# Performance work log

Measured on AMD Instinct MI355X. Metric: run time of the kernel, lower is better.

The kernel has to match this reference:

```python
import jax, jax.numpy as jnp
import numpy as np

N_USERS = 70000
N_ITEMS = 30000
N_NODES = N_USERS + N_ITEMS
R = 3          # n_relations (hard-coded to 3 in original forward)
D = 64         # emb_dim
L = 2          # n_layers
E = 1_600_000  # nnz per relation adjacency


def setup_inputs() -> dict:
    key = jax.random.key(0)
    ks = jax.random.split(key, 11)
    s = 0.05  # xavier-ish scale
    return {
        'user_emb': jax.random.normal(ks[0], (N_USERS, D), jnp.float32) * s,
        'item_emb': jax.random.normal(ks[1], (N_ITEMS, D), jnp.float32) * s,
        'rel_emb':  jax.random.normal(ks[2], (R, D), jnp.float32) * s,
        'W_gc':     jax.random.normal(ks[3], (L, D, D), jnp.float32) * s,
        'W_rel':    jax.random.normal(ks[4], (L, D, D), jnp.float32) * s,
        'gru_w':    jax.random.normal(ks[5], (R, D, D), jnp.float32) * s,
        'gru_b':    jax.random.normal(ks[6], (R, D), jnp.float32) * s,
        'tra':      jax.random.normal(ks[7], (2, 2 * D), jnp.float32) * s,
        # normalized sparse adjacency values (~1/degree)
        'adj_vals': jax.random.uniform(ks[8], (R, E), jnp.float32) / 16.0,
        'adj_rows': jax.random.randint(ks[9], (R, E), 0, N_NODES, dtype=jnp.int32),
        'adj_cols': jax.random.randint(ks[10], (R, E), 0, N_NODES, dtype=jnp.int32),
    }


def reference(user_emb, item_emb, rel_emb, W_gc, W_rel, gru_w, gru_b, tra,
              adj_vals, adj_rows, adj_cols):
    # ego: [N, R, D] (same embedding replicated per relation channel)
    ego = jnp.broadcast_to(
        jnp.concatenate([user_emb, item_emb], axis=0)[:, None, :],
        (N_NODES, R, D))
    all_emb = ego
    rela = [rel_emb]  # per-layer relation embeddings [R, D]
    inv_sqrt = 1.0 / jnp.sqrt(jnp.float32(128.0))  # hard-coded in source

    for k in range(L):
        embs = []
        for i in range(R):  # small fixed relation loop
            # sparse adj @ ego[:, i, :] via gather + segment_sum
            msgs = ego[adj_cols[i], i, :] * adj_vals[i][:, None]        # [E, D]
            prop = jax.ops.segment_sum(msgs, adj_rows[i],
                                       num_segments=N_NODES)           # [N, D]
            embs.append(jax.nn.leaky_relu((prop * rela[k][i]) @ W_gc[k]))
        est = jnp.stack(embs, axis=1)                                   # [N, R, D]
        att = jax.nn.softmax(
            jnp.einsum('nrd,nsd->nrs', est, est) * inv_sqrt, axis=2)
        ego = jnp.einsum('nrs,nsd->nrd', att, est)
        # dropout rate 0.0 (eval) -> identity
        all_emb = all_emb + ego
        rela.append(rela[k] @ W_rel[k])

    att = jax.nn.softmax(jnp.einsum('nrd,nsd->nrs', all_emb, all_emb), axis=2)
    mid = jnp.einsum('nrs,nsd->nrd', att, all_emb)
    final = jnp.stack([all_emb[:, 0, :], all_emb[:, 1, :], mid[:, -1, :]],
                      axis=1) / (L + 1)                                  # [N, 3, D]
    u = final[:N_USERS]
    i_emb = jnp.concatenate(
        [final[N_USERS:], jnp.zeros((1, R, D), final.dtype)], axis=0)

    aux1 = u[:, 0, :] * (u[:, 0, :] @ gru_w[0] + gru_b[0])
    aux2 = u[:, 1, :] * (u[:, 1, :] @ gru_w[1] + gru_b[1])
    tgt = u[:, 2, :] * (u[:, 2, :] @ gru_w[2] + gru_b[2])
    score1 = jnp.concatenate([tgt, aux1], axis=1) @ tra[0]               # [N_u]
    score2 = jnp.concatenate([tgt, aux2], axis=1) @ tra[1]               # [N_u]

    rela_out = jnp.mean(jnp.stack(rela, axis=0), axis=0)                 # [R, D]
    return (u, i_emb, rela_out, score1, score2)
```

## Files before the change

### kernel.cpp

```cpp
#include <hip/hip_runtime.h>
#include <hip/hip_bf16.h>

#define N_USERS 70000
#define N_ITEMS 30000
#define N_NODES 100000
#define RD 192
#define EE 1600000
#define NE3 4800000
#define M3 300000
#define NSUB 98
#define NBUCK 294

#define OFF_U    0
#define OFF_I    13440000
#define OFF_IZ   19200000
#define OFF_RELA 19200192
#define OFF_S1   19200384
#define OFF_S2   19270384

typedef __hip_bfloat16 bf16;
typedef unsigned long long u64;
typedef __attribute__((ext_vector_type(8))) short short8;
typedef __attribute__((ext_vector_type(8))) unsigned short ushort8;
typedef __attribute__((ext_vector_type(4))) float f32x4;

__device__ __forceinline__ float b2f(bf16 v) { return __bfloat162float(v); }

union bfbits { bf16 b; unsigned short u; };

__device__ __forceinline__ float bits2f(unsigned short u) {
  bfbits x; x.u = u; return b2f(x.b);
}
__device__ __forceinline__ unsigned short f2bits(float f) {
  bfbits x; x.b = __float2bfloat16(f); return x.u;
}

__device__ __forceinline__ float loadf(const void* p, int i, bool f32) {
  return f32 ? ((const float*)p)[i] : b2f(((const bf16*)p)[i]);
}
__device__ __forceinline__ void storef(void* p, int i, float v, bool f32) {
  if (f32) ((float*)p)[i] = v;
  else ((bf16*)p)[i] = __float2bfloat16(v);
}

template <int NV>
__device__ __forceinline__ void wave_sum_n(float* v) {
#pragma unroll
  for (int off = 32; off >= 1; off >>= 1) {
    float t[NV];
#pragma unroll
    for (int k = 0; k < NV; ++k) t[k] = __shfl_xor(v[k], off, 64);
#pragma unroll
    for (int k = 0; k < NV; ++k) v[k] += t[k];
  }
}

__global__ void detect_kernel(const unsigned short* __restrict__ ue,
                              int* __restrict__ flag) {
  __shared__ int s;
  int t = threadIdx.x;
  if (t == 0) s = 0;
  __syncthreads();
  int big = 0;
  for (int j = t; j < 8192; j += 256) {
    int e = (ue[j] >> 7) & 0xFF;
    if (e >= 127) big = 1;
  }
  if (big) atomicOr(&s, 1);
  __syncthreads();
  if (t == 0) *flag = s;
}

__global__ void zero_row_kernel(void* out, const int* __restrict__ flag) {
  bool f32 = *flag != 0;
  storef(out, OFF_IZ + (int)threadIdx.x, 0.f, f32);
}

__global__ void rela_kernel(const void* __restrict__ rel_emb,
                            const void* __restrict__ W_rel,
                            const int* __restrict__ flag,
                            float* __restrict__ rela_f, void* out) {
  bool f32 = *flag != 0;
  __shared__ float r0s[192], r1s[192];
  int t = threadIdx.x;
  int i = t >> 6, d = t & 63;
  float r0 = loadf(rel_emb, t, f32);
  r0s[t] = r0;
  __syncthreads();
  float acc = 0.f;
  for (int k = 0; k < 64; ++k)
    acc += r0s[i * 64 + k] * loadf(W_rel, k * 64 + d, f32);
  r1s[t] = acc;
  __syncthreads();
  float acc2 = 0.f;
  for (int k = 0; k < 64; ++k)
    acc2 += r1s[i * 64 + k] * loadf(W_rel, 4096 + k * 64 + d, f32);
  rela_f[t] = r0;
  rela_f[192 + t] = acc;
  rela_f[384 + t] = acc2;
  storef(out, OFF_RELA + t, (r0 + acc + acc2) * (1.f / 3.f), f32);
}

__global__ __launch_bounds__(256) void init_kernel(
    const void* __restrict__ user_emb, const void* __restrict__ item_emb,
    const int* __restrict__ flag, bf16* __restrict__ ego0) {
  bool f32 = *flag != 0;
  int idx4 = blockIdx.x * 256 + threadIdx.x;
  if (idx4 >= N_NODES * RD / 4) return;
  int idx = idx4 << 2;
  int n = idx / RD;
  int rd = idx - n * RD;
  int d = rd & 63;
  const void* src;
  int off;
  if (n < N_USERS) { src = user_emb; off = n * 64 + d; }
  else             { src = item_emb; off = (n - N_USERS) * 64 + d; }
  ushort4 o;
  if (f32) {
    float4 fv = *(const float4*)((const float*)src + off);
    o.x = f2bits(fv.x); o.y = f2bits(fv.y); o.z = f2bits(fv.z); o.w = f2bits(fv.w);
  } else {
    o = *(const ushort4*)((const unsigned short*)src + off);
  }
  *(ushort4*)(ego0 + idx) = o;
}

__global__ __launch_bounds__(256) void bhist_kernel(
    const int* __restrict__ rows, int* __restrict__ bcnt) {
  __shared__ int h[NBUCK];
  int t = threadIdx.x;
  for (int j = t; j < NBUCK; j += 256) h[j] = 0;
  __syncthreads();
  int base = blockIdx.x * 4096;
  int m = min(4096, NE3 - base);
  for (int j = t; j < m; j += 256) {
    int idx = base + j;
    int i = idx / EE;
    int r = rows[idx];
    atomicAdd(&h[i * NSUB + (r >> 10)], 1);
  }
  __syncthreads();
  for (int j = t; j < NBUCK; j += 256)
    if (h[j]) atomicAdd(&bcnt[j], h[j]);
}

__global__ __launch_bounds__(512) void bscan_kernel(
    const int* __restrict__ bcnt, int* __restrict__ gcursor,
    int* __restrict__ bbase) {
  __shared__ int s[512];
  int t = threadIdx.x;
  int x = (t < NBUCK) ? bcnt[t] : 0;
  s[t] = x;
  __syncthreads();
  for (int off = 1; off < 512; off <<= 1) {
    int y = (t >= off) ? s[t - off] : 0;
    __syncthreads();
    s[t] += y;
    __syncthreads();
  }
  if (t < NBUCK) {
    int e = s[t] - x;
    gcursor[t] = e;
    bbase[t] = e;
  }
}

__global__ __launch_bounds__(256) void passA_kernel(
    const int* __restrict__ rows, const int* __restrict__ cols,
    const void* __restrict__ vals, const int* __restrict__ flag,
    int* __restrict__ gcursor, u64* __restrict__ abuf) {
  bool f32 = *flag != 0;
  __shared__ u64 pk[4096];
  __shared__ unsigned short bk[4096];
  __shared__ int cnt[NBUCK], pos[NBUCK], gbase[NBUCK];
  int t = threadIdx.x;
  for (int j = t; j < NBUCK; j += 256) { cnt[j] = 0; pos[j] = 0; }
  __syncthreads();
  int base = blockIdx.x * 4096;
  int m = min(4096, NE3 - base);
  for (int j = t; j < m; j += 256) {
    int idx = base + j;
    int i = idx / EE;
    int r = rows[idx];
    int c = cols[idx];
    unsigned short vb =
        f32 ? f2bits(((const float*)vals)[idx])
            : ((const unsigned short*)vals)[idx];
    int sub = r >> 10;
    int b = i * NSUB + sub;
    pk[j] = ((u64)(r & 1023) << 48) | ((u64)(unsigned)c << 16) | vb;
    bk[j] = (unsigned short)b;
    atomicAdd(&cnt[b], 1);
  }
  __syncthreads();
  for (int j = t; j < NBUCK; j += 256)
    if (cnt[j] > 0) gbase[j] = atomicAdd(&gcursor[j], cnt[j]);
  __syncthreads();
  for (int j = t; j < m; j += 256) {
    int b = bk[j];
    int p = atomicAdd(&pos[b], 1);
    abuf[gbase[b] + p] = pk[j];
  }
}

__global__ __launch_bounds__(256) void passB_kernel(
    const u64* __restrict__ abuf, const int* __restrict__ bbase,
    const int* __restrict__ bcnt, int* __restrict__ offs,
    int* __restrict__ counts, int2* __restrict__ sedge) {
  __shared__ int hist[1024];
  __shared__ int s[256];
  int b = blockIdx.x;
  int rel = b / NSUB, sub = b - rel * NSUB;
  int r0 = sub << 10;
  int nr = min(1024, N_NODES - r0);
  int gi = rel * N_NODES + r0;
  int t = threadIdx.x;
  for (int j = t; j < 1024; j += 256) hist[j] = 0;
  __syncthreads();
  int start = bbase[b];
  int cnt = bcnt[b];
  int end = start + cnt;
  for (int e = start + t; e < end; e += 256)
    atomicAdd(&hist[(int)(abuf[e] >> 48)], 1);
  __syncthreads();
  int j0 = t << 2;
  int a0 = hist[j0], a1 = hist[j0 + 1], a2 = hist[j0 + 2], a3 = hist[j0 + 3];
  int lsum = a0 + a1 + a2 + a3;
  s[t] = lsum;
  __syncthreads();
  for (int off = 1; off < 256; off <<= 1) {
    int y = (t >= off) ? s[t - off] : 0;
    __syncthreads();
    s[t] += y;
    __syncthreads();
  }
  int o0 = start + s[t] - lsum;
  int o1 = o0 + a0, o2 = o1 + a1, o3 = o2 + a2;
  hist[j0] = o0; hist[j0 + 1] = o1; hist[j0 + 2] = o2; hist[j0 + 3] = o3;
  if (j0 < nr) {
    *(int4*)(offs + gi + j0) = make_int4(o0, o1, o2, o3);
    *(int4*)(counts + gi + j0) = make_int4(a0, a1, a2, a3);
  }
  __syncthreads();
  int rbase = rel * 128;
  for (int e = start + t; e < end; e += 256) {
    u64 w = abuf[e];
    int rowlo = (int)(w >> 48);
    int c = (int)((w >> 16) & 0x3FFFF);
    float v = bits2f((unsigned short)(w & 0xFFFF));
    int p = atomicAdd(&hist[rowlo], 1);
    int2 eo; eo.x = c * 384 + rbase; eo.y = __float_as_int(v);
    sedge[p] = eo;
  }
}

__global__ __launch_bounds__(256, 8) void gather_kernel(
    const int2* __restrict__ sedge, const int* __restrict__ counts,
    const int* __restrict__ offs, const bf16* __restrict__ ego,
    bf16* __restrict__ prop) {
  int wave = threadIdx.x >> 6;
  int n = blockIdx.x * 4 + wave;
  int rel = blockIdx.y;
  int seg = rel * N_NODES + n;
  int lane = threadIdx.x & 63;
  int g = lane >> 3;
  int d8 = lane & 7;
  unsigned voff = (unsigned)(d8 << 4);
  int base = __builtin_amdgcn_readfirstlane(offs[seg]);
  int cnt = __builtin_amdgcn_readfirstlane(counts[seg]);
  const char* egob = (const char*)ego;
  float a0 = 0.f, a1 = 0.f, a2 = 0.f, a3 = 0.f;
  float a4 = 0.f, a5 = 0.f, a6 = 0.f, a7 = 0.f;
#define ACCUM(dv, vv)                                          \
  do {                                                         \
    a0 = fmaf(__int_as_float((dv).x << 16), (vv), a0);         \
    a1 = fmaf(__int_as_float((dv).x & 0xffff0000u), (vv), a1); \
    a2 = fmaf(__int_as_float((dv).y << 16), (vv), a2);         \
    a3 = fmaf(__int_as_float((dv).y & 0xffff0000u), (vv), a3); \
    a4 = fmaf(__int_as_float((dv).z << 16), (vv), a4);         \
    a5 = fmaf(__int_as_float((dv).z & 0xffff0000u), (vv), a5); \
    a6 = fmaf(__int_as_float((dv).w << 16), (vv), a6);         \
    a7 = fmaf(__int_as_float((dv).w & 0xffff0000u), (vv), a7); \
  } while (0)
  int cm = cnt - 1;
  int nb = (cnt + 15) >> 4;
  int j = 0;
  if (nb & 1) {
    int iA = min(g, cm), iB = min(8 + g, cm);
    int2 h0 = sedge[base + iA];
    int2 h1 = sedge[base + iB];
    uint4 dA = *(const uint4*)(egob + ((unsigned)h0.x + voff));
    uint4 dB = *(const uint4*)(egob + ((unsigned)h1.x + voff));
    float v0 = (g < cnt) ? __int_as_float(h0.y) : 0.f;
    float v1 = (8 + g < cnt) ? __int_as_float(h1.y) : 0.f;
    ACCUM(dA, v0);
    ACCUM(dB, v1);
    j = 16;
  }
  int e16 = nb << 4;
  for (; j < e16; j += 32) {
    int iA0 = min(j + g, cm),      iB0 = min(j + 8 + g, cm);
    int iA1 = min(j + 16 + g, cm), iB1 = min(j + 24 + g, cm);
    int2 h0a = sedge[base + iA0];
    int2 h1a = sedge[base + iB0];
    int2 h0b = sedge[base + iA1];
    int2 h1b = sedge[base + iB1];
    uint4 dA = *(const uint4*)(egob + ((unsigned)h0a.x + voff));
    uint4 dB = *(const uint4*)(egob + ((unsigned)h1a.x + voff));
    uint4 dC = *(const uint4*)(egob + ((unsigned)h0b.x + voff));
    uint4 dD = *(const uint4*)(egob + ((unsigned)h1b.x + voff));
    float v0 = (j + g < cnt) ? __int_as_float(h0a.y) : 0.f;
    float v1 = (j + 8 + g < cnt) ? __int_as_float(h1a.y) : 0.f;
    float v2 = (j + 16 + g < cnt) ? __int_as_float(h0b.y) : 0.f;
    float v3 = (j + 24 + g < cnt) ? __int_as_float(h1b.y) : 0.f;
    ACCUM(dA, v0);
    ACCUM(dB, v1);
    ACCUM(dC, v2);
    ACCUM(dD, v3);
  }
#undef ACCUM
#pragma unroll
  for (int off = 8; off <= 32; off <<= 1) {
    a0 += __shfl_xor(a0, off, 64);
    a1 += __shfl_xor(a1, off, 64);
    a2 += __shfl_xor(a2, off, 64);
    a3 += __shfl_xor(a3, off, 64);
    a4 += __shfl_xor(a4, off, 64);
    a5 += __shfl_xor(a5, off, 64);
    a6 += __shfl_xor(a6, off, 64);
    a7 += __shfl_xor(a7, off, 64);
  }
  if (g == 0) {
    uint4 o;
    o.x = (unsigned)f2bits(a0) | ((unsigned)f2bits(a1) << 16);
    o.y = (unsigned)f2bits(a2) | ((unsigned)f2bits(a3) << 16);
    o.z = (unsigned)f2bits(a4) | ((unsigned)f2bits(a5) << 16);
    o.w = (unsigned)f2bits(a6) | ((unsigned)f2bits(a7) << 16);
    *(uint4*)((char*)prop + (size_t)(n * RD + rel * 64) * 2 + voff) = o;
  }
}

__device__ __forceinline__ float attn_row(float a, float b, float c,
                                          float e0, float e1, float e2) {
  float m = fmaxf(a, fmaxf(b, c));
  float w0 = __expf(a - m), w1 = __expf(b - m), w2 = __expf(c - m);
  float inv = 1.f / (w0 + w1 + w2);
  return (w0 * e0 + w1 * e1 + w2 * e2) * inv;
}

__global__ __launch_bounds__(256, 4) void transform_attn_kernel(
    const bf16* __restrict__ prop, const float* __restrict__ rela_k,
    const void* __restrict__ Wgc, int wgc_off, const int* __restrict__ flag,
    bf16* __restrict__ ego_out) {
  bool f32 = *flag != 0;
  __shared__ __align__(16) unsigned short est_t[64 * 198];
  int t = threadIdx.x, lane = t & 63, wave = t >> 6;
  int quad = lane >> 4, m = lane & 15;
  int wcol = wave * 16 + m;
  short8 b0, b1;
#pragma unroll
  for (int j = 0; j < 8; ++j) {
    int k0 = quad * 8 + j;
    b0[j] = (short)f2bits(loadf(Wgc, wgc_off + k0 * 64 + wcol, f32));
    b1[j] = (short)f2bits(loadf(Wgc, wgc_off + (k0 + 32) * 64 + wcol, f32));
  }
  float relv0[16], relv1[16], relv2[16];
#pragma unroll
  for (int j = 0; j < 8; ++j) {
    int k0 = quad * 8 + j;
    relv0[j] = rela_k[k0];        relv0[8 + j] = rela_k[32 + k0];
    relv1[j] = rela_k[64 + k0];   relv1[8 + j] = rela_k[96 + k0];
    relv2[j] = rela_k[128 + k0];  relv2[8 + j] = rela_k[160 + k0];
  }
  int n0 = blockIdx.x * 64;
  int row0 = n0 * 3;
#pragma unroll
  for (int tr = 0; tr < 12; ++tr) {
    int rl = tr * 16 + m;
    int row = row0 + rl;
    int row_c = row < M3 ? row : 0;
    int i = rl % 3;
    const ushort8* pp = (const ushort8*)(prop + (size_t)row_c * 64 + quad * 8);
    ushort8 x0 = pp[0];
    ushort8 x1 = pp[4];
    short8 a0, a1;
#pragma unroll
    for (int j = 0; j < 8; ++j) {
      float r0 = (i == 0) ? relv0[j] : (i == 1 ? relv1[j] : relv2[j]);
      float r1 = (i == 0) ? relv0[8 + j] : (i == 1 ? relv1[8 + j] : relv2[8 + j]);
      a0[j] = (short)f2bits(bits2f(x0[j]) * r0);
      a1[j] = (short)f2bits(bits2f(x1[j]) * r1);
    }
    f32x4 acc = {0.f, 0.f, 0.f, 0.f};
    acc = __builtin_amdgcn_mfma_f32_16x16x32_bf16(a0, b0, acc, 0, 0, 0);
    acc = __builtin_amdgcn_mfma_f32_16x16x32_bf16(a1, b1, acc, 0, 0, 0);
    float v0 = acc[0]; v0 = v0 > 0.f ? v0 : 0.01f * v0;
    float v1 = acc[1]; v1 = v1 > 0.f ? v1 : 0.01f * v1;
    float v2 = acc[2]; v2 = v2 > 0.f ? v2 : 0.01f * v2;
    float v3 = acc[3]; v3 = v3 > 0.f ? v3 : 0.01f * v3;
    unsigned w0 = (unsigned)f2bits(v0) | ((unsigned)f2bits(v1) << 16);
    unsigned w1 = (unsigned)f2bits(v2) | ((unsigned)f2bits(v3) << 16);
    unsigned* p32 = (unsigned*)(est_t + wcol * 198 + tr * 16 + quad * 4);
    p32[0] = w0; p32[1] = w1;
  }
  __syncthreads();
  const float sc = 0.088388347648318447f;
  for (int jj = 0; jj < 16; ++jj) {
    int nl = wave * 16 + jj;
    int n = n0 + nl;
    if (n >= N_NODES) break;
    int rb = lane * 198 + 3 * nl;
    float e0 = bits2f(est_t[rb]);
    float e1 = bits2f(est_t[rb + 1]);
    float e2 = bits2f(est_t[rb + 2]);
    float s[6];
    s[0] = e0 * e0; s[1] = e0 * e1; s[2] = e0 * e2;
    s[3] = e1 * e1; s[4] = e1 * e2; s[5] = e2 * e2;
    wave_sum_n<6>(s);
    float o0 = attn_row(s[0] * sc, s[1] * sc, s[2] * sc, e0, e1, e2);
    float o1 = attn_row(s[1] * sc, s[3] * sc, s[4] * sc, e0, e1, e2);
    float o2 = attn_row(s[2] * sc, s[4] * sc, s[5] * sc, e0, e1, e2);
    int base = n * RD + lane;
    ego_out[base] = __float2bfloat16(o0);
    ego_out[base + 64] = __float2bfloat16(o1);
    ego_out[base + 128] = __float2bfloat16(o2);
  }
}

__global__ __launch_bounds__(256, 5) void final_kernel(
    const bf16* __restrict__ ego0, const bf16* __restrict__ ego1,
    const bf16* __restrict__ ego2, const void* __restrict__ gru_w,
    const void* __restrict__ gru_b, const void* __restrict__ tra,
    const int* __restrict__ flag, void* out) {
  bool f32 = *flag != 0;
  __shared__ __align__(16) unsigned short fmatu[192 * 72];
  __shared__ float sc_lds[128];
  int t = threadIdx.x, lane = t & 63, wave = t >> 6;
  int quad = lane >> 4, m = lane & 15;
  int wcol = wave * 16 + m;
  if (t < 128) sc_lds[t] = 0.f;
  short8 bw[3][2];
#pragma unroll
  for (int i = 0; i < 3; ++i)
#pragma unroll
    for (int j = 0; j < 8; ++j) {
      int k0 = quad * 8 + j;
      bw[i][0][j] = (short)f2bits(loadf(gru_w, i * 4096 + k0 * 64 + wcol, f32));
      bw[i][1][j] =
          (short)f2bits(loadf(gru_w, i * 4096 + (k0 + 32) * 64 + wcol, f32));
    }
  float bias0 = loadf(gru_b, wcol, f32);
  float bias1 = loadf(gru_b, 64 + wcol, f32);
  float bias2 = loadf(gru_b, 128 + wcol, f32);
  float ts0 = loadf(tra, wcol, f32);
  float ts1 = loadf(tra, 64 + wcol, f32);
  float ts2 = loadf(tra, 128 + wcol, f32);
  float ts3 = loadf(tra, 192 + wcol, f32);

  int n0 = blockIdx.x * 64;
  for (int jj = 0; jj < 16; jj += 2) {
    int nlA = wave * 16 + jj;
    int nlB = nlA + 1;
    int nA = n0 + nlA, nB = n0 + nlB;
    float a0A = 0.f, a1A = 0.f, a2A = 0.f;
    float a0B = 0.f, a1B = 0.f, a2B = 0.f;
    if (nA < N_NODES) {
      int bi = nA * RD + lane;
      a0A = b2f(ego0[bi]) + b2f(ego1[bi]) + b2f(ego2[bi]);
      a1A = b2f(ego0[bi + 64]) + b2f(ego1[bi + 64]) + b2f(ego2[bi + 64]);
      a2A = b2f(ego0[bi + 128]) + b2f(ego1[bi + 128]) + b2f(ego2[bi + 128]);
    }
    if (nB < N_NODES) {
      int bi = nB * RD + lane;
      a0B = b2f(ego0[bi]) + b2f(ego1[bi]) + b2f(ego2[bi]);
      a1B = b2f(ego0[bi + 64]) + b2f(ego1[bi + 64]) + b2f(ego2[bi + 64]);
      a2B = b2f(ego0[bi + 128]) + b2f(ego1[bi + 128]) + b2f(ego2[bi + 128]);
    }
    float s[6];
    s[0] = a2A * a0A; s[1] = a2A * a1A; s[2] = a2A * a2A;
    s[3] = a2B * a0B; s[4] = a2B * a1B; s[5] = a2B * a2B;
    wave_sum_n<6>(s);
    float mid2A = attn_row(s[0], s[1], s[2], a0A, a1A, a2A);
    float mid2B = attn_row(s[3], s[4], s[5], a0B, a1B, a2B);
    float f0A = a0A * (1.f / 3.f), f1A = a1A * (1.f / 3.f),
          f2A = mid2A * (1.f / 3.f);
    float f0B = a0B * (1.f / 3.f), f1B = a1B * (1.f / 3.f),
          f2B = mid2B * (1.f / 3.f);
    if (nA < N_NODES) {
      int ob = (nA < N_USERS) ? (OFF_U + nA * RD + lane)
                              : (OFF_I + (nA - N_USERS) * RD + lane);
      storef(out, ob, f0A, f32);
      storef(out, ob + 64, f1A, f32);
      storef(out, ob + 128, f2A, f32);
    }
    if (nB < N_NODES) {
      int ob = (nB < N_USERS) ? (OFF_U + nB * RD + lane)
                              : (OFF_I + (nB - N_USERS) * RD + lane);
      storef(out, ob, f0B, f32);
      storef(out, ob + 64, f1B, f32);
      storef(out, ob + 128, f2B, f32);
    }
    fmatu[(0 * 64 + nlA) * 72 + lane] = f2bits(f0A);
    fmatu[(1 * 64 + nlA) * 72 + lane] = f2bits(f1A);
    fmatu[(2 * 64 + nlA) * 72 + lane] = f2bits(f2A);
    fmatu[(0 * 64 + nlB) * 72 + lane] = f2bits(f0B);
    fmatu[(1 * 64 + nlB) * 72 + lane] = f2bits(f1B);
    fmatu[(2 * 64 + nlB) * 72 + lane] = f2bits(f2B);
  }
  __syncthreads();
  float p1a[4][4], p2a[4][4];
#pragma unroll
  for (int tr = 0; tr < 4; ++tr)
#pragma unroll
    for (int r = 0; r < 4; ++r) { p1a[tr][r] = 0.f; p2a[tr][r] = 0.f; }
#pragma unroll
  for (int i = 0; i < 3; ++i) {
    float bias = (i == 0) ? bias0 : (i == 1 ? bias1 : bias2);
#pragma unroll
    for (int tr = 0; tr < 4; ++tr) {
      int arow = (i * 64 + tr * 16 + m) * 72;
      short8 a0 = *(const short8*)(fmatu + arow + quad * 8);
      short8 a1 = *(const short8*)(fmatu + arow + 32 + quad * 8);
      f32x4 acc = {0.f, 0.f, 0.f, 0.f};
      acc = __builtin_amdgcn_mfma_f32_16x16x32_bf16(a0, bw[i][0], acc, 0, 0, 0);
      acc = __builtin_amdgcn_mfma_f32_16x16x32_bf16(a1, bw[i][1], acc, 0, 0, 0);
#pragma unroll
      for (int r = 0; r < 4; ++r) {
        int nl = tr * 16 + quad * 4 + r;
        float y = acc[r] + bias;
        float f = bits2f(fmatu[(i * 64 + nl) * 72 + wcol]);
        float prod = f * y;
        if (i == 0) p1a[tr][r] += prod * ts1;
        else if (i == 1) p2a[tr][r] += prod * ts3;
        else { p1a[tr][r] += prod * ts0; p2a[tr][r] += prod * ts2; }
      }
    }
  }
#pragma unroll
  for (int tr = 0; tr < 4; ++tr)
#pragma unroll
    for (int r = 0; r < 4; ++r) {
      float p1 = p1a[tr][r], p2 = p2a[tr][r];
#pragma unroll
      for (int off = 1; off < 16; off <<= 1) {
        p1 += __shfl_xor(p1, off, 64);
        p2 += __shfl_xor(p2, off, 64);
      }
      if (m == 0) {
        int nl = tr * 16 + quad * 4 + r;
        atomicAdd(&sc_lds[nl * 2], p1);
        atomicAdd(&sc_lds[nl * 2 + 1], p2);
      }
    }
  __syncthreads();
  if (t < 64) {
    int n = n0 + t;
    if (n < N_USERS) {
      storef(out, OFF_S1 + n, sc_lds[t * 2], f32);
      storef(out, OFF_S2 + n, sc_lds[t * 2 + 1], f32);
    }
  }
}

extern "C" void kernel_launch(void* const* d_in, const int* in_sizes, int n_in,
                              void* d_out, int out_size, void* d_ws,
                              size_t ws_size, hipStream_t stream) {
  const void* user_emb = d_in[0];
  const void* item_emb = d_in[1];
  const void* rel_emb = d_in[2];
  const void* W_gc = d_in[3];
  const void* W_rel = d_in[4];
  const void* gru_w = d_in[5];
  const void* gru_b = d_in[6];
  const void* tra = d_in[7];
  const void* adj_vals = d_in[8];
  const int* adj_rows = (const int*)d_in[9];
  const int* adj_cols = (const int*)d_in[10];

  int* flag = (int*)d_ws;
  float* wsf = (float*)d_ws;
  float* rela_f = wsf + 16;
  int* counts = (int*)(wsf + 1024);
  int* offs = counts + M3;
  int* gcursor = offs + M3;
  int* bcnt = gcursor + 512;
  int* bbase = bcnt + 512;
  u64* abuf = (u64*)(bbase + 512);
  int2* sedge = (int2*)(abuf + NE3);
  bf16* ego0 = (bf16*)(sedge + NE3);
  bf16* ego1 = ego0 + (size_t)N_NODES * RD;
  bf16* ego2 = ego1 + (size_t)N_NODES * RD;
  bf16* prop = ego2 + (size_t)N_NODES * RD;

  const int nbE = (NE3 + 4095) / 4096;

  detect_kernel<<<1, 256, 0, stream>>>((const unsigned short*)user_emb, flag);
  rela_kernel<<<1, 192, 0, stream>>>(rel_emb, W_rel, flag, rela_f, d_out);
  zero_row_kernel<<<1, 192, 0, stream>>>(d_out, flag);
  init_kernel<<<(N_NODES * RD / 4 + 255) / 256, 256, 0, stream>>>(
      user_emb, item_emb, flag, ego0);

  (void)hipMemsetAsync(bcnt, 0, 512 * sizeof(int), stream);
  bhist_kernel<<<nbE, 256, 0, stream>>>(adj_rows, bcnt);
  bscan_kernel<<<1, 512, 0, stream>>>(bcnt, gcursor, bbase);
  passA_kernel<<<nbE, 256, 0, stream>>>(
      adj_rows, adj_cols, adj_vals, flag, gcursor, abuf);
  passB_kernel<<<NBUCK, 256, 0, stream>>>(abuf, bbase, bcnt, offs, counts,
                                          sedge);

  gather_kernel<<<dim3(N_NODES / 4, 3), 256, 0, stream>>>(
      sedge, counts, offs, ego0, prop);
  transform_attn_kernel<<<(N_NODES + 63) / 64, 256, 0, stream>>>(
      prop, rela_f, W_gc, 0, flag, ego1);
  gather_kernel<<<dim3(N_NODES / 4, 3), 256, 0, stream>>>(
      sedge, counts, offs, ego1, prop);
  transform_attn_kernel<<<(N_NODES + 63) / 64, 256, 0, stream>>>(
      prop, rela_f + 192, W_gc, 4096, flag, ego2);

  final_kernel<<<(N_NODES + 63) / 64, 256, 0, stream>>>(
      ego0, ego1, ego2, gru_w, gru_b, tra, flag, d_out);
}
```

Baseline: 738.0 us.

## Fold relation scale into weights, restructure MFMA tiling, fuse layer sum into transform

Folds the per-relation scale rela_k into the W_gc fragments, precomputing one weight fragment per relation so the per-element multiply on prop disappears. Prop rows are now loaded per node per relation channel as direct MFMA operands. The second transform kernel also adds ego0 and ego1 to its output, so final_kernel reads one summed buffer instead of three. Launch bounds rise to 6 waves per SIMD. Folding the scale into bf16 weights changes rounding, and the scattered 16-bit LDS stores may add bank traffic.

```diff
diff --git a/kernel.cpp b/kernel.cpp
--- a/kernel.cpp
+++ b/kernel.cpp
@@ -348,60 +348,49 @@
   return (w0 * e0 + w1 * e1 + w2 * e2) * inv;
 }
 
-__global__ __launch_bounds__(256, 4) void transform_attn_kernel(
+__global__ __launch_bounds__(256, 6) void transform_attn_kernel(
     const bf16* __restrict__ prop, const float* __restrict__ rela_k,
     const void* __restrict__ Wgc, int wgc_off, const int* __restrict__ flag,
+    const bf16* __restrict__ add0, const bf16* __restrict__ add1,
     bf16* __restrict__ ego_out) {
   bool f32 = *flag != 0;
   __shared__ __align__(16) unsigned short est_t[64 * 198];
   int t = threadIdx.x, lane = t & 63, wave = t >> 6;
   int quad = lane >> 4, m = lane & 15;
   int wcol = wave * 16 + m;
-  short8 b0, b1;
-#pragma unroll
-  for (int j = 0; j < 8; ++j) {
-    int k0 = quad * 8 + j;
-    b0[j] = (short)f2bits(loadf(Wgc, wgc_off + k0 * 64 + wcol, f32));
-    b1[j] = (short)f2bits(loadf(Wgc, wgc_off + (k0 + 32) * 64 + wcol, f32));
-  }
-  float relv0[16], relv1[16], relv2[16];
-#pragma unroll
-  for (int j = 0; j < 8; ++j) {
-    int k0 = quad * 8 + j;
-    relv0[j] = rela_k[k0];        relv0[8 + j] = rela_k[32 + k0];
-    relv1[j] = rela_k[64 + k0];   relv1[8 + j] = rela_k[96 + k0];
-    relv2[j] = rela_k[128 + k0];  relv2[8 + j] = rela_k[160 + k0];
-  }
+  short8 bw[3][2];
+#pragma unroll
+  for (int i = 0; i < 3; ++i)
+#pragma unroll
+    for (int j = 0; j < 8; ++j) {
+      int k0 = quad * 8 + j;
+      bw[i][0][j] = (short)f2bits(
+          rela_k[i * 64 + k0] * loadf(Wgc, wgc_off + k0 * 64 + wcol, f32));
+      bw[i][1][j] = (short)f2bits(
+          rela_k[i * 64 + k0 + 32] *
+          loadf(Wgc, wgc_off + (k0 + 32) * 64 + wcol, f32));
+    }
   int n0 = blockIdx.x * 64;
-  int row0 = n0 * 3;
-#pragma unroll
-  for (int tr = 0; tr < 12; ++tr) {
-    int rl = tr * 16 + m;
-    int row = row0 + rl;
-    int row_c = row < M3 ? row : 0;
-    int i = rl % 3;
-    const ushort8* pp = (const ushort8*)(prop + (size_t)row_c * 64 + quad * 8);
-    ushort8 x0 = pp[0];
-    ushort8 x1 = pp[4];
-    short8 a0, a1;
-#pragma unroll
-    for (int j = 0; j < 8; ++j) {
-      float r0 = (i == 0) ? relv0[j] : (i == 1 ? relv1[j] : relv2[j]);
-      float r1 = (i == 0) ? relv0[8 + j] : (i == 1 ? relv1[8 + j] : relv2[8 + j]);
-      a0[j] = (short)f2bits(bits2f(x0[j]) * r0);
-      a1[j] = (short)f2bits(bits2f(x1[j]) * r1);
-    }
-    f32x4 acc = {0.f, 0.f, 0.f, 0.f};
-    acc = __builtin_amdgcn_mfma_f32_16x16x32_bf16(a0, b0, acc, 0, 0, 0);
-    acc = __builtin_amdgcn_mfma_f32_16x16x32_bf16(a1, b1, acc, 0, 0, 0);
-    float v0 = acc[0]; v0 = v0 > 0.f ? v0 : 0.01f * v0;
-    float v1 = acc[1]; v1 = v1 > 0.f ? v1 : 0.01f * v1;
-    float v2 = acc[2]; v2 = v2 > 0.f ? v2 : 0.01f * v2;
-    float v3 = acc[3]; v3 = v3 > 0.f ? v3 : 0.01f * v3;
-    unsigned w0 = (unsigned)f2bits(v0) | ((unsigned)f2bits(v1) << 16);
-    unsigned w1 = (unsigned)f2bits(v2) | ((unsigned)f2bits(v3) << 16);
-    unsigned* p32 = (unsigned*)(est_t + wcol * 198 + tr * 16 + quad * 4);
-    p32[0] = w0; p32[1] = w1;
+#pragma unroll
+  for (int i = 0; i < 3; ++i) {
+#pragma unroll
+    for (int nt = 0; nt < 4; ++nt) {
+      int node = n0 + nt * 16 + m;
+      if (node > N_NODES - 1) node = N_NODES - 1;
+      const short8* pp =
+          (const short8*)(prop + (size_t)node * RD + i * 64 + quad * 8);
+      short8 x0 = pp[0];
+      short8 x1 = pp[4];
+      f32x4 acc = {0.f, 0.f, 0.f, 0.f};
+      acc = __builtin_amdgcn_mfma_f32_16x16x32_bf16(x0, bw[i][0], acc, 0, 0, 0);
+      acc = __builtin_amdgcn_mfma_f32_16x16x32_bf16(x1, bw[i][1], acc, 0, 0, 0);
+#pragma unroll
+      for (int r = 0; r < 4; ++r) {
+        float v = acc[r];
+        v = v > 0.f ? v : 0.01f * v;
+        est_t[wcol * 198 + 3 * (nt * 16 + quad * 4 + r) + i] = f2bits(v);
+      }
+    }
   }
   __syncthreads();
   const float sc = 0.088388347648318447f;
@@ -409,6 +398,13 @@
     int nl = wave * 16 + jj;
     int n = n0 + nl;
     if (n >= N_NODES) break;
+    int base = n * RD + lane;
+    float g0 = 0.f, g1 = 0.f, g2 = 0.f;
+    if (add0) {
+      g0 = b2f(add0[base]) + b2f(add1[base]);
+      g1 = b2f(add0[base + 64]) + b2f(add1[base + 64]);
+      g2 = b2f(add0[base + 128]) + b2f(add1[base + 128]);
+    }
     int rb = lane * 198 + 3 * nl;
     float e0 = bits2f(est_t[rb]);
     float e1 = bits2f(est_t[rb + 1]);
@@ -420,16 +416,14 @@
     float o0 = attn_row(s[0] * sc, s[1] * sc, s[2] * sc, e0, e1, e2);
     float o1 = attn_row(s[1] * sc, s[3] * sc, s[4] * sc, e0, e1, e2);
     float o2 = attn_row(s[2] * sc, s[4] * sc, s[5] * sc, e0, e1, e2);
-    int base = n * RD + lane;
-    ego_out[base] = __float2bfloat16(o0);
-    ego_out[base + 64] = __float2bfloat16(o1);
-    ego_out[base + 128] = __float2bfloat16(o2);
+    ego_out[base] = __float2bfloat16(o0 + g0);
+    ego_out[base + 64] = __float2bfloat16(o1 + g1);
+    ego_out[base + 128] = __float2bfloat16(o2 + g2);
   }
 }
 
 __global__ __launch_bounds__(256, 5) void final_kernel(
-    const bf16* __restrict__ ego0, const bf16* __restrict__ ego1,
-    const bf16* __restrict__ ego2, const void* __restrict__ gru_w,
+    const bf16* __restrict__ asum, const void* __restrict__ gru_w,
     const void* __restrict__ gru_b, const void* __restrict__ tra,
     const int* __restrict__ flag, void* out) {
   bool f32 = *flag != 0;
@@ -466,15 +460,15 @@
     float a0B = 0.f, a1B = 0.f, a2B = 0.f;
     if (nA < N_NODES) {
       int bi = nA * RD + lane;
-      a0A = b2f(ego0[bi]) + b2f(ego1[bi]) + b2f(ego2[bi]);
-      a1A = b2f(ego0[bi + 64]) + b2f(ego1[bi + 64]) + b2f(ego2[bi + 64]);
-      a2A = b2f(ego0[bi + 128]) + b2f(ego1[bi + 128]) + b2f(ego2[bi + 128]);
+      a0A = b2f(asum[bi]);
+      a1A = b2f(asum[bi + 64]);
+      a2A = b2f(asum[bi + 128]);
     }
     if (nB < N_NODES) {
       int bi = nB * RD + lane;
-      a0B = b2f(ego0[bi]) + b2f(ego1[bi]) + b2f(ego2[bi]);
-      a1B = b2f(ego0[bi + 64]) + b2f(ego1[bi + 64]) + b2f(ego2[bi + 64]);
-      a2B = b2f(ego0[bi + 128]) + b2f(ego1[bi + 128]) + b2f(ego2[bi + 128]);
+      a0B = b2f(asum[bi]);
+      a1B = b2f(asum[bi + 64]);
+      a2B = b2f(asum[bi + 128]);
     }
     float s[6];
     s[0] = a2A * a0A; s[1] = a2A * a1A; s[2] = a2A * a2A;
@@ -589,8 +583,8 @@
   int2* sedge = (int2*)(abuf + NE3);
   bf16* ego0 = (bf16*)(sedge + NE3);
   bf16* ego1 = ego0 + (size_t)N_NODES * RD;
-  bf16* ego2 = ego1 + (size_t)N_NODES * RD;
-  bf16* prop = ego2 + (size_t)N_NODES * RD;
+  bf16* asum = ego1 + (size_t)N_NODES * RD;
+  bf16* prop = asum + (size_t)N_NODES * RD;
 
   const int nbE = (NE3 + 4095) / 4096;
 
@@ -611,12 +605,13 @@
   gather_kernel<<<dim3(N_NODES / 4, 3), 256, 0, stream>>>(
       sedge, counts, offs, ego0, prop);
   transform_attn_kernel<<<(N_NODES + 63) / 64, 256, 0, stream>>>(
-      prop, rela_f, W_gc, 0, flag, ego1);
+      prop, rela_f, W_gc, 0, flag, (const bf16*)nullptr, (const bf16*)nullptr,
+      ego1);
   gather_kernel<<<dim3(N_NODES / 4, 3), 256, 0, stream>>>(
       sedge, counts, offs, ego1, prop);
   transform_attn_kernel<<<(N_NODES + 63) / 64, 256, 0, stream>>>(
-      prop, rela_f + 192, W_gc, 4096, flag, ego2);
+      prop, rela_f + 192, W_gc, 4096, flag, ego0, ego1, asum);
 
   final_kernel<<<(N_NODES + 63) / 64, 256, 0, stream>>>(
-      ego0, ego1, ego2, gru_w, gru_b, tra, flag, d_out);
-}
+      asum, gru_w, gru_b, tra, flag, d_out);
+}
```

New measurement: 801.4 us. +8.6%, slower.
